# Kernel tuning notes

Hardware: AMD Instinct MI355X
Metric: run time of the kernel (lower is better)

## Reference

```python
import jax, jax.numpy as jnp
import numpy as np

D, S, E, MPE = 256, 128, 512, 4096
B, N = 2, 4096


def _rope(x):
    # x: (..., n, d); RoPE over axis -2 positions (dim=1 in the torch code)
    n, d = x.shape[-2], x.shape[-1]
    half = d // 2
    pos = jnp.arange(n, dtype=x.dtype)
    inv_freq = 10000.0 ** (-jnp.arange(half, dtype=x.dtype) / half)
    sinusoid = pos[:, None] * inv_freq  # (n, half)
    sin, cos = jnp.sin(sinusoid), jnp.cos(sinusoid)
    x1, x2 = jnp.split(x, 2, axis=-1)
    return jnp.concatenate([x1 * cos - x2 * sin, x2 * cos + x1 * sin], axis=-1)


def setup_inputs() -> dict:
    key = jax.random.key(0)
    ks = jax.random.split(key, 12)
    std = 0.02
    return {
        "query": jax.random.normal(ks[0], (B, N, D), jnp.float32),
        "ln_w": jnp.ones((D,), jnp.float32),
        "ln_b": jnp.zeros((D,), jnp.float32),
        "Wu": jax.random.normal(ks[1], (D, E), jnp.float32) / np.float32(np.sqrt(D)),
        "bu": jnp.zeros((E,), jnp.float32),
        "Wv": jax.random.normal(ks[2], (D, E), jnp.float32) / np.float32(np.sqrt(D)),
        "bv": jnp.zeros((E,), jnp.float32),
        "Wbase": jax.random.normal(ks[3], (D, S), jnp.float32) / np.float32(np.sqrt(D)),
        "bbase": jnp.zeros((S,), jnp.float32),
        "q_w": jax.random.normal(ks[4], (1, S), jnp.float32) * std,
        "q_b": jnp.zeros((1, S), jnp.float32),
        "k_w": jax.random.normal(ks[5], (1, S), jnp.float32) * std,
        "k_b": jnp.zeros((1, S), jnp.float32),
        "w_rel": jax.random.normal(ks[6], (2 * MPE - 1,), jnp.float32) * std,
        "Wo": jax.random.normal(ks[7], (E, D), jnp.float32) / np.float32(np.sqrt(E)),
        "bo": jnp.zeros((D,), jnp.float32),
    }


def reference(query, ln_w, ln_b, Wu, bu, Wv, bv, Wbase, bbase,
              q_w, q_b, k_w, k_b, w_rel, Wo, bo):
    mpe = (w_rel.shape[0] + 1) // 2
    bsz, n, d = query.shape
    # LayerNorm
    mu = query.mean(axis=-1, keepdims=True)
    var = ((query - mu) ** 2).mean(axis=-1, keepdims=True)
    x = (query - mu) * jax.lax.rsqrt(var + 1e-5) * ln_w + ln_b
    # gated projections
    u = jax.nn.silu(x @ Wu + bu)       # (B,N,E)
    v = jax.nn.silu(x @ Wv + bv)       # (B,N,E)
    base = jax.nn.silu(x @ Wbase + bbase)  # (B,N,S)
    q = _rope(base * q_w + q_b)
    k = _rope(base * k_w + k_b)
    qk = jnp.einsum('bms,bns->bmn', q, k)  # (B,N,N)
    # Toeplitz relative-position bias: bias[i,j] = w_rel[mpe-1 + j - i]
    # (equivalent to the torch pad/repeat/reshape construction, sliced to n)
    i = jnp.arange(n)
    bias = w_rel[(mpe - 1) + i[None, :] - i[:, None]]  # (N,N)
    kernel = jnp.square(jax.nn.relu(qk / mpe + bias))
    out = (u * jnp.einsum('bmn,bne->bme', kernel, v)) @ Wo + bo
    return out
```

## Files before the change

### kernel.cpp

```cpp
#include <hip/hip_runtime.h>
#include <hip/hip_bf16.h>
#include <math.h>

typedef __bf16 bf16_8 __attribute__((ext_vector_type(8)));
typedef float f32x4 __attribute__((ext_vector_type(4)));
typedef float f32x16 __attribute__((ext_vector_type(16)));

#define D_ 256
#define S_ 128
#define E_ 512
#define MPE_ 4096
#define B_ 2
#define N_ 4096
#define M_TOT (B_*N_)

__device__ __forceinline__ ushort f2b(float f) {
  union { float f; uint u; } x; x.f = f;
  uint r = (x.u + 0x7FFFu + ((x.u >> 16) & 1u)) >> 16;
  return (ushort)r;
}
__device__ __forceinline__ float b2f(ushort b) {
  union { uint u; float f; } x; x.u = ((uint)b) << 16;
  return x.f;
}

__device__ __forceinline__ void gl_lds16(const void* g, void* l) {
  __builtin_amdgcn_global_load_lds(
      (const __attribute__((address_space(1))) void*)g,
      (__attribute__((address_space(3))) void*)l, 16, 0, 0);
}

__global__ __launch_bounds__(256) void ln_kernel(const float* __restrict__ q,
    const float* __restrict__ w, const float* __restrict__ b,
    ushort* __restrict__ x) {
  int wid = threadIdx.x >> 6, lane = threadIdx.x & 63;
  int row = blockIdx.x * 4 + wid;
  const float* qr = q + (size_t)row * D_;
  float4 v = *(const float4*)(qr + lane * 4);
  float s  = v.x + v.y + v.z + v.w;
  float ss = v.x*v.x + v.y*v.y + v.z*v.z + v.w*v.w;
  #pragma unroll
  for (int off = 32; off; off >>= 1) {
    s  += __shfl_xor(s, off);
    ss += __shfl_xor(ss, off);
  }
  float mu   = s * (1.0f / 256.0f);
  float var  = ss * (1.0f / 256.0f) - mu * mu;
  float rstd = rsqrtf(var + 1e-5f);
  ushort4 o;
  float vv[4] = {v.x, v.y, v.z, v.w};
  ushort ot[4];
  #pragma unroll
  for (int j = 0; j < 4; ++j) {
    int c = lane * 4 + j;
    ot[j] = f2b((vv[j] - mu) * rstd * w[c] + b[c]);
  }
  o.x = ot[0]; o.y = ot[1]; o.z = ot[2]; o.w = ot[3];
  *(ushort4*)(x + (size_t)row * D_ + lane * 4) = o;
}

__global__ void wt_kernel(const float* __restrict__ in, ushort* __restrict__ out,
                          int R, int C) {
  int o = blockIdx.x * 256 + threadIdx.x;
  if (o >= R * C) return;
  int c = o / R, r = o - c * R;
  out[o] = f2b(in[r * C + c]);
}

__global__ __launch_bounds__(256) void wrep_kernel(const float* __restrict__ w_rel,
                                                   float* __restrict__ wrep) {
  int idx = blockIdx.x * 256 + threadIdx.x;
  int c = idx >> 13, i = idx & 8191;
  int s = i + c; if (s > 8190) s = 8190;
  wrep[idx] = w_rel[s];
}

template<int EPI>
__global__ __launch_bounds__(256) void gemm_kernel(
    const ushort* __restrict__ A, const ushort* __restrict__ Bt,
    const float* __restrict__ bias, void* __restrict__ out,
    int M, int N, int K) {
  __shared__ alignas(16) ushort As[128 * 64];
  __shared__ alignas(16) ushort Bs[64 * 64];
  int tid = threadIdx.x;
  int lane = tid & 63, wid = tid >> 6;
  int m0 = blockIdx.x * 128, n0 = blockIdx.y * 64;
  int r16 = lane & 15, kq = lane >> 4;
  f32x4 acc[2][4] = {};
  for (int k0 = 0; k0 < K; k0 += 64) {
    __syncthreads();
    #pragma unroll
    for (int t = 0; t < 4; ++t) {
      int cid = tid + t * 256;
      int row = cid >> 3, c = cid & 7;
      uint4 d = *(const uint4*)(A + ((size_t)(m0 + row) * K + k0 + c * 8));
      *(uint4*)&As[row * 64 + ((c ^ (row & 7)) * 8)] = d;
    }
    #pragma unroll
    for (int t = 0; t < 2; ++t) {
      int cid = tid + t * 256;
      int row = cid >> 3, c = cid & 7;
      uint4 d = *(const uint4*)(Bt + ((size_t)(n0 + row) * K + k0 + c * 8));
      *(uint4*)&Bs[row * 64 + ((c ^ (row & 7)) * 8)] = d;
    }
    __syncthreads();
    #pragma unroll
    for (int ks = 0; ks < 2; ++ks) {
      bf16_8 af[2], bfr[4];
      int c = ks * 4 + kq;
      #pragma unroll
      for (int fm = 0; fm < 2; ++fm) {
        int r = wid * 32 + fm * 16 + r16;
        af[fm] = *(const bf16_8*)&As[r * 64 + ((c ^ (r & 7)) * 8)];
      }
      #pragma unroll
      for (int fn = 0; fn < 4; ++fn) {
        int r = fn * 16 + r16;
        bfr[fn] = *(const bf16_8*)&Bs[r * 64 + ((c ^ (r & 7)) * 8)];
      }
      #pragma unroll
      for (int fm = 0; fm < 2; ++fm)
        #pragma unroll
        for (int fn = 0; fn < 4; ++fn)
          acc[fm][fn] = __builtin_amdgcn_mfma_f32_16x16x32_bf16(af[fm], bfr[fn], acc[fm][fn], 0, 0, 0);
    }
  }
  #pragma unroll
  for (int fm = 0; fm < 2; ++fm)
    #pragma unroll
    for (int fn = 0; fn < 4; ++fn)
      #pragma unroll
      for (int reg = 0; reg < 4; ++reg) {
        int ml = wid * 32 + fm * 16 + kq * 4 + reg;
        int nl = fn * 16 + r16;
        size_t gm = m0 + ml, gn = n0 + nl;
        float val = acc[fm][fn][reg] + bias[gn];
        if (EPI == 0) {
          float y = val / (1.0f + expf(-val));
          ((ushort*)out)[gm * N + gn] = f2b(y);
        } else if (EPI == 2) {
          float y = val / (1.0f + expf(-val));
          ((ushort*)out)[gn * (size_t)M_TOT + gm] = f2b(y);
        } else {
          ((float*)out)[gm * N + gn] = val;
        }
      }
}

__global__ __launch_bounds__(256) void rope_kernel(const ushort* __restrict__ base,
    const float* __restrict__ qw, const float* __restrict__ qb,
    const float* __restrict__ kw, const float* __restrict__ kb,
    ushort* __restrict__ Q, ushort* __restrict__ Kk) {
  int g = blockIdx.x * 256 + threadIdx.x;
  int row = g >> 6, i = g & 63;
  int n = row & (N_ - 1);
  float invf = powf(10000.0f, -(float)i * (1.0f / 64.0f));
  float sv, cv;
  sincosf((float)n * invf, &sv, &cv);
  const float sc = 0.015625f;
  float b1 = b2f(base[row * S_ + i]), b2 = b2f(base[row * S_ + 64 + i]);
  float x1q = b1 * qw[i] + qb[i], x2q = b2 * qw[64 + i] + qb[64 + i];
  Q[row * S_ + i]      = f2b((x1q * cv - x2q * sv) * sc);
  Q[row * S_ + 64 + i] = f2b((x2q * cv + x1q * sv) * sc);
  float x1k = b1 * kw[i] + kb[i], x2k = b2 * kw[64 + i] + kb[64 + i];
  Kk[row * S_ + i]      = f2b((x1k * cv - x2k * sv) * sc);
  Kk[row * S_ + 64 + i] = f2b((x2k * cv + x1k * sv) * sc);
}

__global__ __launch_bounds__(512, 2) void attn_kernel(
    const ushort* __restrict__ Q, const ushort* __restrict__ Kd,
    const ushort* __restrict__ VT, const ushort* __restrict__ U,
    const float* __restrict__ wrep, ushort* __restrict__ KVU) {
  __shared__ alignas(16) ushort SM[32768];
  char* SMc = (char*)&SM[0];
  const int tid = threadIdx.x, lane = tid & 63, wid = tid >> 6;
  const int wg = wid >> 1, nh = wid & 1;
  const int b = blockIdx.z, m0 = blockIdx.x * 128, e0 = blockIdx.y * 128;
  const int l31 = lane & 31, hi = lane >> 5;
  const int mrow = m0 + wg * 32 + l31;

  const int bbase = 4095 + 32 * nh + 4 * hi - mrow;
  const int csel = bbase & 3;
  const float* wrow = wrep + csel * 8192 + (bbase - csel);

  bf16_8 qf[8];
  #pragma unroll
  for (int ks = 0; ks < 8; ++ks)
    qf[ks] = *(const bf16_8*)(Q + ((size_t)(b * N_ + mrow) * S_ + ks * 16 + hi * 8));

  auto stage_k = [&](int bi, int nt) {
    int n0s = nt * 64;
    #pragma unroll
    for (int tt = 0; tt < 2; ++tt) {
      int p = tt * 512 + tid;
      int row = p >> 4, sc2 = p & 15;
      int cc = sc2 ^ (row & 7);
      gl_lds16(Kd + ((size_t)(b * N_ + n0s + row) * S_ + cc * 8),
               SMc + bi * 16384 + (tt * 512 + wid * 64) * 16);
    }
  };
  auto stage_v = [&](int bi, int nt) {
    int n0s = nt * 64;
    #pragma unroll
    for (int tt = 0; tt < 2; ++tt) {
      int p = tt * 512 + tid;
      int er = p >> 3, sc2 = p & 7;
      int nc = sc2 ^ (er & 7);
      gl_lds16(VT + ((size_t)(e0 + er) * M_TOT + b * N_ + n0s + nc * 8),
               SMc + 32768 + bi * 16384 + (tt * 512 + wid * 64) * 16);
    }
  };

  f32x16 acc[4] = {};
  uint4 paA[2], paB[2];

  auto do_pv = [&](int vb, const uint4 (&paR)[2]) {
    const char* vsb = SMc + 32768 + vb * 16384;
    __builtin_amdgcn_s_setprio(1);
    #pragma unroll
    for (int kb = 0; kb < 2; ++kb) {
      bf16_8 pa = *(const bf16_8*)&paR[kb];
      #pragma unroll
      for (int et = 0; et < 4; ++et) {
        int e = et * 32 + l31;
        int slot = (4 * nh + 2 * kb + hi) ^ (e & 7);
        bf16_8 vf = *(const bf16_8*)(vsb + e * 128 + slot * 16);
        acc[et] = __builtin_amdgcn_mfma_f32_32x32x16_bf16(pa, vf, acc[et], 0, 0, 0);
      }
    }
    __builtin_amdgcn_s_setprio(0);
  };

  auto body = [&](int t, int cur, uint4 (&paW)[2], const uint4 (&paR)[2],
                  bool doPV, bool doK) {
    float4 bb[4];
    #pragma unroll
    for (int rg = 0; rg < 4; ++rg)
      bb[rg] = *(const float4*)(wrow + 64 * t + 8 * rg);
    if (doK) stage_k(cur ^ 1, t + 1);
    stage_v(cur, t);
    __builtin_amdgcn_sched_barrier(0);
    const char* ksb = SMc + cur * 16384;
    f32x16 s0 = {};
    __builtin_amdgcn_s_setprio(1);
    #pragma unroll
    for (int ks = 0; ks < 8; ++ks) {
      int row = nh * 32 + l31;
      int slot = (2 * ks + hi) ^ (l31 & 7);
      bf16_8 kf = *(const bf16_8*)(ksb + row * 256 + slot * 16);
      s0 = __builtin_amdgcn_mfma_f32_32x32x16_bf16(kf, qf[ks], s0, 0, 0, 0);
    }
    __builtin_amdgcn_s_setprio(0);
    if (doPV) do_pv(cur ^ 1, paR);
    uint w0[4], w1[4];
    #pragma unroll
    for (int rg = 0; rg < 4; ++rg) {
      float4 b4 = bb[rg];
      float t0 = fmaxf(s0[4*rg+0] + b4.x, 0.f); t0 *= t0;
      float t1 = fmaxf(s0[4*rg+1] + b4.y, 0.f); t1 *= t1;
      float t2 = fmaxf(s0[4*rg+2] + b4.z, 0.f); t2 *= t2;
      float t3 = fmaxf(s0[4*rg+3] + b4.w, 0.f); t3 *= t3;
      asm("v_cvt_pk_bf16_f32 %0, %1, %2" : "=v"(w0[rg]) : "v"(t0), "v"(t1));
      asm("v_cvt_pk_bf16_f32 %0, %1, %2" : "=v"(w1[rg]) : "v"(t2), "v"(t3));
    }
    #pragma unroll
    for (int kb = 0; kb < 2; ++kb) {
      int rs = 2 * kb;
      uint x0 = w0[rs], y0 = w0[rs + 1];
      asm("v_permlane32_swap_b32 %0, %1" : "+v"(x0), "+v"(y0));
      uint x1 = w1[rs], y1 = w1[rs + 1];
      asm("v_permlane32_swap_b32 %0, %1" : "+v"(x1), "+v"(y1));
      uint4 pk; pk.x = x0; pk.y = x1; pk.z = y0; pk.w = y1;
      paW[kb] = pk;
    }
    asm volatile("s_waitcnt vmcnt(0) lgkmcnt(0)" ::: "memory");
    __builtin_amdgcn_s_barrier();
  };

  stage_k(0, 0);
  asm volatile("s_waitcnt vmcnt(0) lgkmcnt(0)" ::: "memory");
  __builtin_amdgcn_s_barrier();

  body(0, 0, paA, paB, false, true);
  for (int t2 = 0; t2 < 31; ++t2) {
    body(2 * t2 + 1, 1, paB, paA, true, true);
    body(2 * t2 + 2, 0, paA, paB, true, true);
  }
  body(63, 1, paB, paA, true, false);
  do_pv(1, paB);

  __syncthreads();
  float* red = (float*)&SM[0];
  if (nh == 1) {
    #pragma unroll
    for (int et = 0; et < 4; ++et)
      #pragma unroll
      for (int rg4 = 0; rg4 < 4; ++rg4) {
        float4 w;
        w.x = acc[et][4*rg4+0]; w.y = acc[et][4*rg4+1];
        w.z = acc[et][4*rg4+2]; w.w = acc[et][4*rg4+3];
        *(float4*)&red[wg * 4096 + et * 1024 + rg4 * 256 + lane * 4] = w;
      }
  }
  __syncthreads();
  if (nh == 0) {
    #pragma unroll
    for (int et = 0; et < 4; ++et)
      #pragma unroll
      for (int rg4 = 0; rg4 < 4; ++rg4) {
        float4 r = *(const float4*)&red[wg * 4096 + et * 1024 + rg4 * 256 + lane * 4];
        acc[et][4*rg4+0] += r.x; acc[et][4*rg4+1] += r.y;
        acc[et][4*rg4+2] += r.z; acc[et][4*rg4+3] += r.w;
      }
    #pragma unroll
    for (int et = 0; et < 4; ++et)
      #pragma unroll
      for (int reg = 0; reg < 16; ++reg) {
        int ml = (reg & 3) + 8 * (reg >> 2) + 4 * hi;
        size_t grow = (size_t)b * N_ + m0 + wg * 32 + ml;
        size_t ge = e0 + et * 32 + l31;
        float uu = b2f(U[grow * E_ + ge]);
        KVU[grow * E_ + ge] = f2b(uu * acc[et][reg]);
      }
  }
}

extern "C" void kernel_launch(void* const* d_in, const int* in_sizes, int n_in,
                              void* d_out, int out_size, void* d_ws, size_t ws_size,
                              hipStream_t stream) {
  const float* query = (const float*)d_in[0];
  const float* ln_w  = (const float*)d_in[1];
  const float* ln_b  = (const float*)d_in[2];
  const float* Wu    = (const float*)d_in[3];
  const float* bu    = (const float*)d_in[4];
  const float* Wv    = (const float*)d_in[5];
  const float* bv    = (const float*)d_in[6];
  const float* Wbase = (const float*)d_in[7];
  const float* bbase = (const float*)d_in[8];
  const float* q_w   = (const float*)d_in[9];
  const float* q_b   = (const float*)d_in[10];
  const float* k_w   = (const float*)d_in[11];
  const float* k_b   = (const float*)d_in[12];
  const float* w_rel = (const float*)d_in[13];
  const float* Wo    = (const float*)d_in[14];
  const float* bo    = (const float*)d_in[15];
  float* out = (float*)d_out;

  char* ws = (char*)d_ws;
  ushort* X    = (ushort*)(ws);
  ushort* U    = (ushort*)(ws + (4u  << 20));
  ushort* VT   = (ushort*)(ws + (12u << 20));
  ushort* BASE = (ushort*)(ws + (20u << 20));
  ushort* Qb   = (ushort*)(ws + (22u << 20));
  ushort* Kb   = (ushort*)(ws + (24u << 20));
  ushort* KVU  = (ushort*)(ws + (26u << 20));
  ushort* WUT  = (ushort*)(ws + (34u << 20));
  ushort* WVT  = (ushort*)(ws + (34u << 20) + 512*256*2);
  ushort* WBT  = (ushort*)(ws + (34u << 20) + 2*512*256*2);
  ushort* WOT  = (ushort*)(ws + (34u << 20) + 2*512*256*2 + 128*256*2);
  float*  WREP = (float*)(ws);

  ln_kernel<<<2048, 256, 0, stream>>>(query, ln_w, ln_b, X);
  wt_kernel<<<(512*256 + 255) / 256, 256, 0, stream>>>(Wu, WUT, 256, 512);
  wt_kernel<<<(512*256 + 255) / 256, 256, 0, stream>>>(Wv, WVT, 256, 512);
  wt_kernel<<<(128*256 + 255) / 256, 256, 0, stream>>>(Wbase, WBT, 256, 128);
  wt_kernel<<<(512*256 + 255) / 256, 256, 0, stream>>>(Wo, WOT, 512, 256);
  gemm_kernel<0><<<dim3(64, 8), 256, 0, stream>>>(X, WUT, bu, U, 8192, 512, 256);
  gemm_kernel<2><<<dim3(64, 8), 256, 0, stream>>>(X, WVT, bv, VT, 8192, 512, 256);
  gemm_kernel<0><<<dim3(64, 2), 256, 0, stream>>>(X, WBT, bbase, BASE, 8192, 128, 256);
  wrep_kernel<<<128, 256, 0, stream>>>(w_rel, WREP);
  rope_kernel<<<2048, 256, 0, stream>>>(BASE, q_w, q_b, k_w, k_b, Qb, Kb);
  attn_kernel<<<dim3(32, 4, 2), 512, 0, stream>>>(Qb, Kb, VT, U, WREP, KVU);
  gemm_kernel<1><<<dim3(64, 4), 256, 0, stream>>>(KVU, WOT, bo, out, 8192, 256, 512);
}
```

Baseline: 171.2 us.

## Pre-swizzle K/V into MFMA fragment layout and deepen attention pipeline to four buffers

The rope and V-projection epilogues now write K and V directly in per-lane MFMA fragment order, so the attention kernel stages tiles with contiguous 16-byte loads and reads LDS fragments without XOR swizzles. The attention loop moves to four LDS buffers with prefetch two tiles ahead and a partial vmcnt wait instead of a full drain. It also seeds the QK accumulator with the bias and merges the weight-transpose and wrep kernels into one prep launch. The cost is doubled LDS use (128 KB per block, which may limit occupancy) and scattered global writes in the producer epilogues.

```diff
diff --git a/kernel.cpp b/kernel.cpp
--- a/kernel.cpp
+++ b/kernel.cpp
@@ -59,20 +59,32 @@
   *(ushort4*)(x + (size_t)row * D_ + lane * 4) = o;
 }
 
-__global__ void wt_kernel(const float* __restrict__ in, ushort* __restrict__ out,
-                          int R, int C) {
-  int o = blockIdx.x * 256 + threadIdx.x;
-  if (o >= R * C) return;
-  int c = o / R, r = o - c * R;
-  out[o] = f2b(in[r * C + c]);
-}
-
-__global__ __launch_bounds__(256) void wrep_kernel(const float* __restrict__ w_rel,
-                                                   float* __restrict__ wrep) {
-  int idx = blockIdx.x * 256 + threadIdx.x;
-  int c = idx >> 13, i = idx & 8191;
-  int s = i + c; if (s > 8190) s = 8190;
-  wrep[idx] = w_rel[s];
+__global__ __launch_bounds__(256) void prep_kernel(
+    const float* __restrict__ Wu, const float* __restrict__ Wv,
+    const float* __restrict__ Wb, const float* __restrict__ Wo,
+    const float* __restrict__ w_rel,
+    ushort* __restrict__ WUT, ushort* __restrict__ WVT,
+    ushort* __restrict__ WBT, ushort* __restrict__ WOT,
+    float* __restrict__ wrep) {
+  int blk = blockIdx.x, tid = threadIdx.x;
+  if (blk < 512) {
+    int o = blk * 256 + tid; int c = o >> 8, r = o & 255;
+    WUT[o] = f2b(Wu[r * 512 + c]);
+  } else if (blk < 1024) {
+    int o = (blk - 512) * 256 + tid; int c = o >> 8, r = o & 255;
+    WVT[o] = f2b(Wv[r * 512 + c]);
+  } else if (blk < 1152) {
+    int o = (blk - 1024) * 256 + tid; int c = o >> 8, r = o & 255;
+    WBT[o] = f2b(Wb[r * 128 + c]);
+  } else if (blk < 1664) {
+    int o = (blk - 1152) * 256 + tid; int c = o >> 9, r = o & 511;
+    WOT[o] = f2b(Wo[r * 256 + c]);
+  } else {
+    int idx = (blk - 1664) * 256 + tid;
+    int c = idx >> 13, i = idx & 8191;
+    int s = i + c; if (s > 8190) s = 8190;
+    wrep[idx] = w_rel[s];
+  }
 }
 
 template<int EPI>
@@ -140,7 +152,14 @@
           ((ushort*)out)[gm * N + gn] = f2b(y);
         } else if (EPI == 2) {
           float y = val / (1.0f + expf(-val));
-          ((ushort*)out)[gn * (size_t)M_TOT + gm] = f2b(y);
+          int bb = (int)(gm >> 12), n = (int)(gm & 4095);
+          int t = n >> 6, nn = n & 63;
+          int nh = nn >> 5, nl2 = nn & 31;
+          int kb2 = nl2 >> 4, hi = (nl2 >> 3) & 1, j = nl2 & 7;
+          int eb = (int)(gn >> 5), l31e = (int)(gn & 31);
+          size_t addr = ((((size_t)(bb * 64 + t) * 2 + nh) * 2 + kb2) * 16 + eb) * 512
+                      + (hi * 32 + l31e) * 8 + j;
+          ((ushort*)out)[addr] = f2b(y);
         } else {
           ((float*)out)[gm * N + gn] = val;
         }
@@ -149,8 +168,8 @@
 
 __global__ __launch_bounds__(256) void rope_kernel(const ushort* __restrict__ base,
     const float* __restrict__ qw, const float* __restrict__ qb,
-    const float* __restrict__ kw, const float* __restrict__ kb,
-    ushort* __restrict__ Q, ushort* __restrict__ Kk) {
+    const float* __restrict__ kw, const float* __restrict__ kb_,
+    ushort* __restrict__ Q, ushort* __restrict__ KF) {
   int g = blockIdx.x * 256 + threadIdx.x;
   int row = g >> 6, i = g & 63;
   int n = row & (N_ - 1);
@@ -162,52 +181,50 @@
   float x1q = b1 * qw[i] + qb[i], x2q = b2 * qw[64 + i] + qb[64 + i];
   Q[row * S_ + i]      = f2b((x1q * cv - x2q * sv) * sc);
   Q[row * S_ + 64 + i] = f2b((x2q * cv + x1q * sv) * sc);
-  float x1k = b1 * kw[i] + kb[i], x2k = b2 * kw[64 + i] + kb[64 + i];
-  Kk[row * S_ + i]      = f2b((x1k * cv - x2k * sv) * sc);
-  Kk[row * S_ + 64 + i] = f2b((x2k * cv + x1k * sv) * sc);
+  float x1k = b1 * kw[i] + kb_[i], x2k = b2 * kw[64 + i] + kb_[64 + i];
+  float k1 = (x1k * cv - x2k * sv) * sc;
+  float k2 = (x2k * cv + x1k * sv) * sc;
+  int bb = row >> 12, t = n >> 6, nn = n & 63;
+  int nh = nn >> 5, l31 = nn & 31;
+  int kb1 = i >> 4, hi1 = (i >> 3) & 1, j1 = i & 7;
+  size_t fb = (size_t)((bb * 64 + t) * 2 + nh) * 8;
+  KF[(fb + kb1) * 512 + (hi1 * 32 + l31) * 8 + j1] = f2b(k1);
+  KF[(fb + 4 + kb1) * 512 + (hi1 * 32 + l31) * 8 + j1] = f2b(k2);
 }
 
 __global__ __launch_bounds__(512, 2) void attn_kernel(
-    const ushort* __restrict__ Q, const ushort* __restrict__ Kd,
-    const ushort* __restrict__ VT, const ushort* __restrict__ U,
+    const ushort* __restrict__ Q, const ushort* __restrict__ KF,
+    const ushort* __restrict__ VF, const ushort* __restrict__ U,
     const float* __restrict__ wrep, ushort* __restrict__ KVU) {
-  __shared__ alignas(16) ushort SM[32768];
-  char* SMc = (char*)&SM[0];
+  __shared__ alignas(16) ushort SMEM_[65536];
   const int tid = threadIdx.x, lane = tid & 63, wid = tid >> 6;
   const int wg = wid >> 1, nh = wid & 1;
   const int b = blockIdx.z, m0 = blockIdx.x * 128, e0 = blockIdx.y * 128;
   const int l31 = lane & 31, hi = lane >> 5;
   const int mrow = m0 + wg * 32 + l31;
 
-  const int bbase = 4095 + 32 * nh + 4 * hi - mrow;
+  const int bbase = 4095 + nh * 32 + 4 * hi - mrow;
   const int csel = bbase & 3;
   const float* wrow = wrep + csel * 8192 + (bbase - csel);
 
   bf16_8 qf[8];
   #pragma unroll
-  for (int ks = 0; ks < 8; ++ks)
-    qf[ks] = *(const bf16_8*)(Q + ((size_t)(b * N_ + mrow) * S_ + ks * 16 + hi * 8));
-
-  auto stage_k = [&](int bi, int nt) {
-    int n0s = nt * 64;
+  for (int kb = 0; kb < 8; ++kb)
+    qf[kb] = *(const bf16_8*)(Q + ((size_t)(b * N_ + mrow) * S_ + kb * 16 + hi * 8));
+
+  auto stage_kv = [&](int bi, int t) {
+    const ushort* ksrc = KF + (size_t)(b * 64 + t) * 8192;
     #pragma unroll
     for (int tt = 0; tt < 2; ++tt) {
-      int p = tt * 512 + tid;
-      int row = p >> 4, sc2 = p & 15;
-      int cc = sc2 ^ (row & 7);
-      gl_lds16(Kd + ((size_t)(b * N_ + n0s + row) * S_ + cc * 8),
-               SMc + bi * 16384 + (tt * 512 + wid * 64) * 16);
-    }
-  };
-  auto stage_v = [&](int bi, int nt) {
-    int n0s = nt * 64;
+      int cb = tt * 8 + wid;
+      gl_lds16(ksrc + cb * 512 + lane * 8, SMEM_ + bi * 8192 + cb * 512);
+    }
     #pragma unroll
     for (int tt = 0; tt < 2; ++tt) {
-      int p = tt * 512 + tid;
-      int er = p >> 3, sc2 = p & 7;
-      int nc = sc2 ^ (er & 7);
-      gl_lds16(VT + ((size_t)(e0 + er) * M_TOT + b * N_ + n0s + nc * 8),
-               SMc + 32768 + bi * 16384 + (tt * 512 + wid * 64) * 16);
+      int f = tt * 8 + wid;
+      int nh2 = f >> 3, kb2 = (f >> 2) & 1, ebl = f & 3;
+      size_t fragidx = (((size_t)(b * 64 + t) * 2 + nh2) * 2 + kb2) * 16 + (e0 >> 5) + ebl;
+      gl_lds16(VF + fragidx * 512 + lane * 8, SMEM_ + 32768 + bi * 8192 + f * 512);
     }
   };
 
@@ -215,51 +232,51 @@
   uint4 paA[2], paB[2];
 
   auto do_pv = [&](int vb, const uint4 (&paR)[2]) {
-    const char* vsb = SMc + 32768 + vb * 16384;
+    const ushort* vsb = SMEM_ + 32768 + vb * 8192;
     __builtin_amdgcn_s_setprio(1);
     #pragma unroll
     for (int kb = 0; kb < 2; ++kb) {
       bf16_8 pa = *(const bf16_8*)&paR[kb];
       #pragma unroll
       for (int et = 0; et < 4; ++et) {
-        int e = et * 32 + l31;
-        int slot = (4 * nh + 2 * kb + hi) ^ (e & 7);
-        bf16_8 vf = *(const bf16_8*)(vsb + e * 128 + slot * 16);
+        bf16_8 vf = *(const bf16_8*)(vsb + (nh * 8 + kb * 4 + et) * 512 + lane * 8);
         acc[et] = __builtin_amdgcn_mfma_f32_32x32x16_bf16(pa, vf, acc[et], 0, 0, 0);
       }
     }
     __builtin_amdgcn_s_setprio(0);
   };
 
-  auto body = [&](int t, int cur, uint4 (&paW)[2], const uint4 (&paR)[2],
-                  bool doPV, bool doK) {
-    float4 bb[4];
+  auto body = [&](int t, int CUR, int PRV, int NXT, uint4 (&paW)[2],
+                  const uint4 (&paR)[2], bool doPV, bool doStage) {
+    float4 b4[4];
     #pragma unroll
     for (int rg = 0; rg < 4; ++rg)
-      bb[rg] = *(const float4*)(wrow + 64 * t + 8 * rg);
-    if (doK) stage_k(cur ^ 1, t + 1);
-    stage_v(cur, t);
+      b4[rg] = *(const float4*)(wrow + 64 * t + 8 * rg);
     __builtin_amdgcn_sched_barrier(0);
-    const char* ksb = SMc + cur * 16384;
-    f32x16 s0 = {};
+    if (doStage) stage_kv(NXT, t + 2);
+    __builtin_amdgcn_sched_barrier(0);
+    const ushort* ksb = SMEM_ + CUR * 8192;
+    f32x16 s0;
+    #pragma unroll
+    for (int rg = 0; rg < 4; ++rg) {
+      s0[4*rg+0] = b4[rg].x; s0[4*rg+1] = b4[rg].y;
+      s0[4*rg+2] = b4[rg].z; s0[4*rg+3] = b4[rg].w;
+    }
     __builtin_amdgcn_s_setprio(1);
     #pragma unroll
-    for (int ks = 0; ks < 8; ++ks) {
-      int row = nh * 32 + l31;
-      int slot = (2 * ks + hi) ^ (l31 & 7);
-      bf16_8 kf = *(const bf16_8*)(ksb + row * 256 + slot * 16);
-      s0 = __builtin_amdgcn_mfma_f32_32x32x16_bf16(kf, qf[ks], s0, 0, 0, 0);
+    for (int kb = 0; kb < 8; ++kb) {
+      bf16_8 kf = *(const bf16_8*)(ksb + (nh * 8 + kb) * 512 + lane * 8);
+      s0 = __builtin_amdgcn_mfma_f32_32x32x16_bf16(kf, qf[kb], s0, 0, 0, 0);
     }
     __builtin_amdgcn_s_setprio(0);
-    if (doPV) do_pv(cur ^ 1, paR);
+    if (doPV) do_pv(PRV, paR);
     uint w0[4], w1[4];
     #pragma unroll
     for (int rg = 0; rg < 4; ++rg) {
-      float4 b4 = bb[rg];
-      float t0 = fmaxf(s0[4*rg+0] + b4.x, 0.f); t0 *= t0;
-      float t1 = fmaxf(s0[4*rg+1] + b4.y, 0.f); t1 *= t1;
-      float t2 = fmaxf(s0[4*rg+2] + b4.z, 0.f); t2 *= t2;
-      float t3 = fmaxf(s0[4*rg+3] + b4.w, 0.f); t3 *= t3;
+      float t0 = fmaxf(s0[4*rg+0], 0.f); t0 *= t0;
+      float t1 = fmaxf(s0[4*rg+1], 0.f); t1 *= t1;
+      float t2 = fmaxf(s0[4*rg+2], 0.f); t2 *= t2;
+      float t3 = fmaxf(s0[4*rg+3], 0.f); t3 *= t3;
       asm("v_cvt_pk_bf16_f32 %0, %1, %2" : "=v"(w0[rg]) : "v"(t0), "v"(t1));
       asm("v_cvt_pk_bf16_f32 %0, %1, %2" : "=v"(w1[rg]) : "v"(t2), "v"(t3));
     }
@@ -273,24 +290,27 @@
       uint4 pk; pk.x = x0; pk.y = x1; pk.z = y0; pk.w = y1;
       paW[kb] = pk;
     }
-    asm volatile("s_waitcnt vmcnt(0) lgkmcnt(0)" ::: "memory");
+    asm volatile("s_waitcnt vmcnt(4)" ::: "memory");
     __builtin_amdgcn_s_barrier();
   };
 
-  stage_k(0, 0);
-  asm volatile("s_waitcnt vmcnt(0) lgkmcnt(0)" ::: "memory");
+  stage_kv(0, 0);
+  stage_kv(1, 1);
+  asm volatile("s_waitcnt vmcnt(4)" ::: "memory");
   __builtin_amdgcn_s_barrier();
 
-  body(0, 0, paA, paB, false, true);
-  for (int t2 = 0; t2 < 31; ++t2) {
-    body(2 * t2 + 1, 1, paB, paA, true, true);
-    body(2 * t2 + 2, 0, paA, paB, true, true);
-  }
-  body(63, 1, paB, paA, true, false);
-  do_pv(1, paB);
+  for (int u = 0; u < 16; ++u) {
+    int t0i = 4 * u;
+    body(t0i,     0, 3, 2, paA, paB, t0i > 0, t0i     <= 61);
+    body(t0i + 1, 1, 0, 3, paB, paA, true,    t0i + 1 <= 61);
+    body(t0i + 2, 2, 1, 0, paA, paB, true,    t0i + 2 <= 61);
+    body(t0i + 3, 3, 2, 1, paB, paA, true,    t0i + 3 <= 61);
+  }
+  asm volatile("s_waitcnt vmcnt(0)" ::: "memory");
+  do_pv(3, paB);
 
   __syncthreads();
-  float* red = (float*)&SM[0];
+  float* red = (float*)SMEM_;
   if (nh == 1) {
     #pragma unroll
     for (int et = 0; et < 4; ++et)
@@ -349,27 +369,24 @@
   char* ws = (char*)d_ws;
   ushort* X    = (ushort*)(ws);
   ushort* U    = (ushort*)(ws + (4u  << 20));
-  ushort* VT   = (ushort*)(ws + (12u << 20));
+  ushort* VF   = (ushort*)(ws + (12u << 20));
   ushort* BASE = (ushort*)(ws + (20u << 20));
   ushort* Qb   = (ushort*)(ws + (22u << 20));
-  ushort* Kb   = (ushort*)(ws + (24u << 20));
+  ushort* KF   = (ushort*)(ws + (24u << 20));
   ushort* KVU  = (ushort*)(ws + (26u << 20));
   ushort* WUT  = (ushort*)(ws + (34u << 20));
   ushort* WVT  = (ushort*)(ws + (34u << 20) + 512*256*2);
   ushort* WBT  = (ushort*)(ws + (34u << 20) + 2*512*256*2);
   ushort* WOT  = (ushort*)(ws + (34u << 20) + 2*512*256*2 + 128*256*2);
-  float*  WREP = (float*)(ws);
+  float*  WREP = (float*)(ws + (35u << 20));
 
   ln_kernel<<<2048, 256, 0, stream>>>(query, ln_w, ln_b, X);
-  wt_kernel<<<(512*256 + 255) / 256, 256, 0, stream>>>(Wu, WUT, 256, 512);
-  wt_kernel<<<(512*256 + 255) / 256, 256, 0, stream>>>(Wv, WVT, 256, 512);
-  wt_kernel<<<(128*256 + 255) / 256, 256, 0, stream>>>(Wbase, WBT, 256, 128);
-  wt_kernel<<<(512*256 + 255) / 256, 256, 0, stream>>>(Wo, WOT, 512, 256);
+  prep_kernel<<<1792, 256, 0, stream>>>(Wu, Wv, Wbase, Wo, w_rel,
+                                        WUT, WVT, WBT, WOT, WREP);
   gemm_kernel<0><<<dim3(64, 8), 256, 0, stream>>>(X, WUT, bu, U, 8192, 512, 256);
-  gemm_kernel<2><<<dim3(64, 8), 256, 0, stream>>>(X, WVT, bv, VT, 8192, 512, 256);
+  gemm_kernel<2><<<dim3(64, 8), 256, 0, stream>>>(X, WVT, bv, VF, 8192, 512, 256);
   gemm_kernel<0><<<dim3(64, 2), 256, 0, stream>>>(X, WBT, bbase, BASE, 8192, 128, 256);
-  wrep_kernel<<<128, 256, 0, stream>>>(w_rel, WREP);
-  rope_kernel<<<2048, 256, 0, stream>>>(BASE, q_w, q_b, k_w, k_b, Qb, Kb);
-  attn_kernel<<<dim3(32, 4, 2), 512, 0, stream>>>(Qb, Kb, VT, U, WREP, KVU);
+  rope_kernel<<<2048, 256, 0, stream>>>(BASE, q_w, q_b, k_w, k_b, Qb, KF);
+  attn_kernel<<<dim3(32, 4, 2), 512, 0, stream>>>(Qb, KF, VF, U, WREP, KVU);
   gemm_kernel<1><<<dim3(64, 4), 256, 0, stream>>>(KVU, WOT, bo, out, 8192, 256, 512);
 }
```

Result: faster. 166.2 us (-2.9%).
